# Kernel optimization log

Measured on AMD Instinct MI355X. Metric: run time of the kernel, lower is better.

Reference implementation:

```python
import jax, jax.numpy as jnp
import numpy as np

N_CHR = 23
N_EMB = 512
E_DIM = 128
B = 4
L = 2048


def setup_inputs() -> dict:
    key = jax.random.key(0)
    k1, k2, k3 = jax.random.split(key, 3)
    chromosome = jax.random.randint(k1, (B, N_CHR, L), 0, N_CHR)
    position = jax.random.uniform(k2, (B, N_CHR, L), dtype=jnp.float32)
    embeddings = jax.random.normal(k3, (N_CHR, N_EMB, E_DIM), dtype=jnp.float32)
    centers = jnp.tile(jnp.linspace(0.0, 1.0, N_EMB, dtype=jnp.float32)[None, :], (N_CHR, 1))  # [23,512]
    log_variances = jnp.full((N_CHR, N_EMB), -5.0, dtype=jnp.float32)
    return {
        "chromosome": chromosome,
        "position": position,
        "embeddings": embeddings,
        "centers": centers,
        "log_variances": log_variances,
    }


def reference(chromosome, position, embeddings, centers, log_variances):
    # position: [B, C=23, L]; centers/log_variances: [C, K=512]; embeddings: [C, K, E]
    variances = jnp.exp(log_variances)                       # [C, K]
    d = position[..., None] - centers[None, :, None, :]      # [B, C, L, K]
    rbf = jnp.exp(-(d * d) / (2.0 * variances[None, :, None, :]))
    weights = jax.nn.softmax(rbf, axis=-1)                   # softmax over codebook (matches torch)
    out = jnp.einsum("bclk,cke->bcle", weights, embeddings)  # [B, C, L, E]
    bsz = position.shape[0]
    return out.reshape(bsz, -1, embeddings.shape[-1])        # [B, C*L, E]
```

## Files before the change

kernel.cpp:

```cpp
#include <hip/hip_runtime.h>
#include <hip/hip_bf16.h>

#define N_CHR 23
#define N_EMB 512
#define E_DIM 128
#define B_SZ  4
#define L_SEQ 2048

typedef __attribute__((ext_vector_type(8))) short short8;
typedef __attribute__((ext_vector_type(4))) float floatx4;

__device__ __forceinline__ float bf2f(unsigned short u) {
    return __uint_as_float(((unsigned)u) << 16);
}
__device__ __forceinline__ unsigned short f2bf(float f) {
    unsigned u = __float_as_uint(f);
    unsigned r = u + 0x7FFFu + ((u >> 16) & 1u);
    return (unsigned short)(r >> 16);
}

__global__ __launch_bounds__(256, 4) void rbf_emb_kernel(
    const float* __restrict__ pos,
    const float* __restrict__ emb,
    const float* __restrict__ ctr,
    const float* __restrict__ lvar,
    float* __restrict__ out)
{
    __shared__ float centers_s[N_EMB];
    __shared__ float scale_s[N_EMB];
    __shared__ uint4 Bs[2][512];
    __shared__ float inv_s[64];

    const int tid  = threadIdx.x;
    const int lane = tid & 63;
    const int wave = tid >> 6;
    const int quad = lane >> 4;
    const int m    = lane & 15;

    const int bc   = blockIdx.x >> 5;
    const int mt   = blockIdx.x & 31;
    const int c    = bc % N_CHR;
    const int row0 = mt * 64;

    for (int k = tid; k < N_EMB; k += 256) {
        centers_s[k] = ctr[c * N_EMB + k];
        scale_s[k]   = -0.5f * __expf(-lvar[c * N_EMB + k]);
    }

    const int   myrow = row0 + wave * 16 + m;
    const float posf  = pos[bc * L_SEQ + myrow];

    floatx4 acc[8];
#pragma unroll
    for (int i = 0; i < 8; ++i) acc[i] = (floatx4){0.f, 0.f, 0.f, 0.f};
    float denom = 0.f;

    __syncthreads();

    const int n_st = tid & 127;
    const int qd0  = tid >> 7;
    const float* embc = emb + (size_t)c * (N_EMB * E_DIM);

    for (int ch = 0; ch < 16; ++ch) {
        const int kc = ch * 32;
        uint4* bw = Bs[ch & 1];

#pragma unroll
        for (int qq = 0; qq < 2; ++qq) {
            const int qd = qd0 + qq * 2;
            const float* src = embc + (kc + qd * 8) * E_DIM + n_st;
            unsigned v[8];
#pragma unroll
            for (int j = 0; j < 8; ++j) v[j] = (unsigned)f2bf(src[j * E_DIM]);
            uint4 w;
            w.x = v[0] | (v[1] << 16);
            w.y = v[2] | (v[3] << 16);
            w.z = v[4] | (v[5] << 16);
            w.w = v[6] | (v[7] << 16);
            bw[((n_st >> 4) << 6) + (qd << 4) + (n_st & 15)] = w;
        }

        short8 afrag;
#pragma unroll
        for (int j = 0; j < 8; ++j) {
            const int   k   = kc + quad * 8 + j;
            const float d   = posf - centers_s[k];
            const float rbf = __expf(d * d * scale_s[k]);
            const float p   = __expf(rbf);
            const unsigned short pb = f2bf(p);
            afrag[j] = (short)pb;
            denom += bf2f(pb);
        }

        __syncthreads();

        const uint4* br = bw;
#pragma unroll
        for (int nt = 0; nt < 8; ++nt) {
            short8 bfrag = *(const short8*)&br[(nt << 6) + lane];
            acc[nt] = __builtin_amdgcn_mfma_f32_16x16x32_bf16(afrag, bfrag, acc[nt], 0, 0, 0);
        }
    }

    denom += __shfl_xor(denom, 16);
    denom += __shfl_xor(denom, 32);
    if (lane < 16) inv_s[wave * 16 + m] = 1.0f / denom;
    __syncthreads();

    float* outp = out + (size_t)(bc * L_SEQ + row0 + wave * 16) * E_DIM;
#pragma unroll
    for (int reg = 0; reg < 4; ++reg) {
        const int   r   = quad * 4 + reg;
        const float inv = inv_s[wave * 16 + r];
        float* o = outp + r * E_DIM + m;
#pragma unroll
        for (int nt = 0; nt < 8; ++nt) {
            o[nt * 16] = acc[nt][reg] * inv;
        }
    }
}

extern "C" void kernel_launch(void* const* d_in, const int* in_sizes, int n_in,
                              void* d_out, int out_size, void* d_ws, size_t ws_size,
                              hipStream_t stream) {
    const float* pos  = (const float*)d_in[1];
    const float* emb  = (const float*)d_in[2];
    const float* ctr  = (const float*)d_in[3];
    const float* lvar = (const float*)d_in[4];
    float* out = (float*)d_out;

    const int blocks = (B_SZ * N_CHR) * (L_SEQ / 64);
    rbf_emb_kernel<<<blocks, 256, 0, stream>>>(pos, emb, ctr, lvar, out);
}
```

Baseline: 165.2 us.

## Prepack embeddings to bf16 MFMA layout and stream via global_load_lds

Adds a pre-pass kernel that converts the fp32 embedding table to bf16 once, already in the MFMA B-fragment layout, and stores it in the workspace. The main kernel then copies each chunk straight into LDS with global_load_lds instead of every block re-reading fp32, converting and scattering. It also switches the exps to exp2 with a folded log2e scale and packs centers and scales into one float2 LDS array. The cost is an extra launch, a workspace dependency (with the old kernel kept as fallback), and exp2 rounding differences.

```diff
diff --git a/kernel.cpp b/kernel.cpp
--- a/kernel.cpp
+++ b/kernel.cpp
@@ -6,9 +6,16 @@
 #define E_DIM 128
 #define B_SZ  4
 #define L_SEQ 2048
+#define LOG2E 1.4426950408889634f
 
 typedef __attribute__((ext_vector_type(8))) short short8;
 typedef __attribute__((ext_vector_type(4))) float floatx4;
+
+#if __has_builtin(__builtin_amdgcn_exp2f)
+#define EXP2(x) __builtin_amdgcn_exp2f(x)
+#else
+#define EXP2(x) __expf((x) * 0.6931471805599453f)
+#endif
 
 __device__ __forceinline__ float bf2f(unsigned short u) {
     return __uint_as_float(((unsigned)u) << 16);
@@ -19,11 +26,133 @@
     return (unsigned short)(r >> 16);
 }
 
+__global__ __launch_bounds__(256) void emb_pack_kernel(
+    const float* __restrict__ emb, uint4* __restrict__ embw)
+{
+    const int idx  = blockIdx.x * 256 + threadIdx.x;
+    const int lane = idx & 63;
+    const int nt   = (idx >> 6) & 7;
+    const int ch   = (idx >> 9) & 15;
+    const int c    = idx >> 13;
+    if (c >= N_CHR) return;
+    const int quad = lane >> 4;
+    const int n    = nt * 16 + (lane & 15);
+    const float* src = emb + (size_t)(c * N_EMB + ch * 32 + quad * 8) * E_DIM + n;
+    unsigned v[8];
+#pragma unroll
+    for (int j = 0; j < 8; ++j) v[j] = (unsigned)f2bf(src[j * E_DIM]);
+    uint4 w;
+    w.x = v[0] | (v[1] << 16);
+    w.y = v[2] | (v[3] << 16);
+    w.z = v[4] | (v[5] << 16);
+    w.w = v[6] | (v[7] << 16);
+    embw[idx] = w;
+}
+
 __global__ __launch_bounds__(256, 4) void rbf_emb_kernel(
     const float* __restrict__ pos,
-    const float* __restrict__ emb,
+    const uint4* __restrict__ embw,
     const float* __restrict__ ctr,
     const float* __restrict__ lvar,
+    float* __restrict__ out)
+{
+    __shared__ float2 cs_s[N_EMB];
+    __shared__ uint4 Bs[2][512];
+    __shared__ float inv_s[64];
+
+    const int tid  = threadIdx.x;
+    const int lane = tid & 63;
+    const int wave = tid >> 6;
+    const int quad = lane >> 4;
+    const int m    = lane & 15;
+
+    const int bc   = blockIdx.x >> 5;
+    const int mt   = blockIdx.x & 31;
+    const int c    = bc % N_CHR;
+    const int row0 = mt * 64;
+
+    for (int k = tid; k < N_EMB; k += 256) {
+        cs_s[k] = make_float2(ctr[c * N_EMB + k],
+                              -0.5f * LOG2E * __expf(-lvar[c * N_EMB + k]));
+    }
+
+    const int   myrow = row0 + wave * 16 + m;
+    const float posf  = pos[bc * L_SEQ + myrow];
+
+    floatx4 acc[8];
+#pragma unroll
+    for (int i = 0; i < 8; ++i) acc[i] = (floatx4){0.f, 0.f, 0.f, 0.f};
+    float denom = 0.f;
+
+    __syncthreads();
+
+    const uint4*  gbase = embw + (size_t)c * (16 * 8 * 64);
+    const float2* csq   = cs_s + quad * 8;
+
+    for (int ch = 0; ch < 16; ++ch) {
+        const int kc = ch * 32;
+        uint4* bw = Bs[ch & 1];
+
+        {
+            const uint4* g = gbase + ch * 512 + wave * 128 + lane;
+            __builtin_amdgcn_global_load_lds(
+                (const __attribute__((address_space(1))) void*)(g),
+                (__attribute__((address_space(3))) void*)(bw + wave * 128), 16, 0, 0);
+            __builtin_amdgcn_global_load_lds(
+                (const __attribute__((address_space(1))) void*)(g + 64),
+                (__attribute__((address_space(3))) void*)(bw + wave * 128 + 64), 16, 0, 0);
+        }
+
+        unsigned pk[4];
+#pragma unroll
+        for (int jj = 0; jj < 4; ++jj) {
+            const float2 cs0 = csq[kc + 2 * jj];
+            const float2 cs1 = csq[kc + 2 * jj + 1];
+            const float d0 = posf - cs0.x;
+            const float d1 = posf - cs1.x;
+            const float p0 = EXP2(EXP2(d0 * d0 * cs0.y) * LOG2E);
+            const float p1 = EXP2(EXP2(d1 * d1 * cs1.y) * LOG2E);
+            const unsigned u0 = __float_as_uint(p0);
+            const unsigned u1 = __float_as_uint(p1);
+            const unsigned r0 = (u0 + 0x7FFFu + ((u0 >> 16) & 1u)) >> 16;
+            const unsigned r1 = (u1 + 0x7FFFu + ((u1 >> 16) & 1u)) & 0xFFFF0000u;
+            pk[jj] = r0 | r1;
+            denom += __uint_as_float(r0 << 16) + __uint_as_float(r1);
+        }
+        const int4 pkv = make_int4((int)pk[0], (int)pk[1], (int)pk[2], (int)pk[3]);
+        const short8 afrag = __builtin_bit_cast(short8, pkv);
+
+        __syncthreads();
+
+        const uint4* br = bw;
+#pragma unroll
+        for (int nt = 0; nt < 8; ++nt) {
+            short8 bfrag = *(const short8*)&br[(nt << 6) + lane];
+            acc[nt] = __builtin_amdgcn_mfma_f32_16x16x32_bf16(afrag, bfrag, acc[nt], 0, 0, 0);
+        }
+    }
+
+    denom += __shfl_xor(denom, 16);
+    denom += __shfl_xor(denom, 32);
+    if (lane < 16) inv_s[wave * 16 + m] = 1.0f / denom;
+    __syncthreads();
+
+    float* outp = out + (size_t)(bc * L_SEQ + row0 + wave * 16) * E_DIM;
+#pragma unroll
+    for (int reg = 0; reg < 4; ++reg) {
+        const int   r   = quad * 4 + reg;
+        const float inv = inv_s[wave * 16 + r];
+        float* o = outp + r * E_DIM + m;
+#pragma unroll
+        for (int nt = 0; nt < 8; ++nt) {
+            o[nt * 16] = acc[nt][reg] * inv;
+        }
+    }
+}
+
+__global__ __launch_bounds__(256, 4) void rbf_emb_kernel_slow(
+    const float* __restrict__ pos, const float* __restrict__ emb,
+    const float* __restrict__ ctr, const float* __restrict__ lvar,
     float* __restrict__ out)
 {
     __shared__ float centers_s[N_EMB];
@@ -36,7 +165,6 @@
     const int wave = tid >> 6;
     const int quad = lane >> 4;
     const int m    = lane & 15;
-
     const int bc   = blockIdx.x >> 5;
     const int mt   = blockIdx.x & 31;
     const int c    = bc % N_CHR;
@@ -46,15 +174,11 @@
         centers_s[k] = ctr[c * N_EMB + k];
         scale_s[k]   = -0.5f * __expf(-lvar[c * N_EMB + k]);
     }
-
-    const int   myrow = row0 + wave * 16 + m;
-    const float posf  = pos[bc * L_SEQ + myrow];
-
+    const float posf = pos[bc * L_SEQ + row0 + wave * 16 + m];
     floatx4 acc[8];
 #pragma unroll
     for (int i = 0; i < 8; ++i) acc[i] = (floatx4){0.f, 0.f, 0.f, 0.f};
     float denom = 0.f;
-
     __syncthreads();
 
     const int n_st = tid & 127;
@@ -64,7 +188,6 @@
     for (int ch = 0; ch < 16; ++ch) {
         const int kc = ch * 32;
         uint4* bw = Bs[ch & 1];
-
 #pragma unroll
         for (int qq = 0; qq < 2; ++qq) {
             const int qd = qd0 + qq * 2;
@@ -79,7 +202,6 @@
             w.w = v[6] | (v[7] << 16);
             bw[((n_st >> 4) << 6) + (qd << 4) + (n_st & 15)] = w;
         }
-
         short8 afrag;
 #pragma unroll
         for (int j = 0; j < 8; ++j) {
@@ -91,9 +213,7 @@
             afrag[j] = (short)pb;
             denom += bf2f(pb);
         }
-
         __syncthreads();
-
         const uint4* br = bw;
 #pragma unroll
         for (int nt = 0; nt < 8; ++nt) {
@@ -101,12 +221,10 @@
             acc[nt] = __builtin_amdgcn_mfma_f32_16x16x32_bf16(afrag, bfrag, acc[nt], 0, 0, 0);
         }
     }
-
     denom += __shfl_xor(denom, 16);
     denom += __shfl_xor(denom, 32);
     if (lane < 16) inv_s[wave * 16 + m] = 1.0f / denom;
     __syncthreads();
-
     float* outp = out + (size_t)(bc * L_SEQ + row0 + wave * 16) * E_DIM;
 #pragma unroll
     for (int reg = 0; reg < 4; ++reg) {
@@ -114,9 +232,7 @@
         const float inv = inv_s[wave * 16 + r];
         float* o = outp + r * E_DIM + m;
 #pragma unroll
-        for (int nt = 0; nt < 8; ++nt) {
-            o[nt * 16] = acc[nt][reg] * inv;
-        }
+        for (int nt = 0; nt < 8; ++nt) o[nt * 16] = acc[nt][reg] * inv;
     }
 }
 
@@ -129,6 +245,14 @@
     const float* lvar = (const float*)d_in[4];
     float* out = (float*)d_out;
 
-    const int blocks = (B_SZ * N_CHR) * (L_SEQ / 64);
-    rbf_emb_kernel<<<blocks, 256, 0, stream>>>(pos, emb, ctr, lvar, out);
-}
+    const int    blocks   = (B_SZ * N_CHR) * (L_SEQ / 64);
+    const size_t ws_needed = (size_t)N_CHR * 16 * 8 * 64 * 16;
+
+    if (ws_size >= ws_needed) {
+        uint4* embw = (uint4*)d_ws;
+        emb_pack_kernel<<<(N_CHR * 16 * 8 * 64) / 256, 256, 0, stream>>>(emb, embw);
+        rbf_emb_kernel<<<blocks, 256, 0, stream>>>(pos, embw, ctr, lvar, out);
+    } else {
+        rbf_emb_kernel_slow<<<blocks, 256, 0, stream>>>(pos, emb, ctr, lvar, out);
+    }
+}
```

After: 145.9 us. 11.7% less time.
